# Kernel optimization log

Hardware: AMD Instinct MI355X
Metric: run time of the kernel (lower is better)

The kernel has to match this reference:

```python
import jax, jax.numpy as jnp
import numpy as np

B, N, S, D, ITERS = 128, 8192, 4, 32, 3
LN_EPS = 1e-5

def _ln(x, g, b):
    m = jnp.mean(x, axis=-1, keepdims=True)
    v = jnp.mean((x - m) ** 2, axis=-1, keepdims=True)
    return (x - m) * jax.lax.rsqrt(v + LN_EPS) * g + b

def setup_inputs() -> dict:
    key = jax.random.key(0)
    ks = jax.random.split(key, 16)
    s = 1.0 / np.sqrt(D)
    return {
        "x": jax.random.normal(ks[0], (B, N, D), jnp.float32),
        "slot_noise": jax.random.normal(ks[1], (B, S, D), jnp.float32),
        "slots_mu": jax.random.normal(ks[2], (1, 1, D), jnp.float32),
        "slots_logsigma": jnp.zeros((1, 1, D), jnp.float32),
        "Wq": jax.random.uniform(ks[3], (D, D), jnp.float32, -s, s),
        "Wk": jax.random.uniform(ks[4], (D, D), jnp.float32, -s, s),
        "Wv": jax.random.uniform(ks[5], (D, D), jnp.float32, -s, s),
        "gru_Wih": jax.random.uniform(ks[6], (3 * D, D), jnp.float32, -s, s),
        "gru_Whh": jax.random.uniform(ks[7], (3 * D, D), jnp.float32, -s, s),
        "gru_bih": jax.random.uniform(ks[8], (3 * D,), jnp.float32, -s, s),
        "gru_bhh": jax.random.uniform(ks[9], (3 * D,), jnp.float32, -s, s),
        "mlp_W1": jax.random.uniform(ks[10], (D, D), jnp.float32, -s, s),
        "mlp_b1": jax.random.uniform(ks[11], (D,), jnp.float32, -s, s),
        "mlp_W2": jax.random.uniform(ks[12], (D, D), jnp.float32, -s, s),
        "mlp_b2": jax.random.uniform(ks[13], (D,), jnp.float32, -s, s),
        "lnx_g": jnp.ones((D,), jnp.float32), "lnx_b": jnp.zeros((D,), jnp.float32),
        "lns_g": jnp.ones((D,), jnp.float32), "lns_b": jnp.zeros((D,), jnp.float32),
        "lnff_g": jnp.ones((D,), jnp.float32), "lnff_b": jnp.zeros((D,), jnp.float32),
    }

def reference(x, slot_noise, slots_mu, slots_logsigma, Wq, Wk, Wv,
              gru_Wih, gru_Whh, gru_bih, gru_bhh,
              mlp_W1, mlp_b1, mlp_W2, mlp_b2,
              lnx_g, lnx_b, lns_g, lns_b, lnff_g, lnff_b):
    d = x.shape[-1]
    scale = d ** (-0.5)
    xn = _ln(x, lnx_g, lnx_b)                      # [B,N,D]
    k = xn @ Wk.T                                  # [B,N,D] (x fixed -> hoist out of loop)
    v = xn @ Wv.T
    slots = slots_mu + slot_noise * jnp.exp(slots_logsigma)  # [B,S,D]
    for _ in range(ITERS):
        q = _ln(slots, lns_g, lns_b) @ Wq.T        # [B,S,D]
        attn = jnp.einsum('bsd,bnd->bsn', q, k) * scale
        attn = jax.nn.softmax(attn, axis=-1) + 1e-8
        attn = attn / jnp.sum(attn, axis=-1, keepdims=True)
        upd = jnp.einsum('bsn,bnd->bsd', attn, v)  # [B,S,D]
        # GRUCell (PyTorch gate order: r, z, n)
        gi = upd @ gru_Wih.T + gru_bih             # [B,S,3D]
        gh = slots @ gru_Whh.T + gru_bhh
        ir, iz, inn = jnp.split(gi, 3, axis=-1)
        hr, hz, hn = jnp.split(gh, 3, axis=-1)
        r = jax.nn.sigmoid(ir + hr)
        z = jax.nn.sigmoid(iz + hz)
        n = jnp.tanh(inn + r * hn)
        slots = (1.0 - z) * n + z * slots
        h = jax.nn.relu(_ln(slots, lnff_g, lnff_b) @ mlp_W1.T + mlp_b1)
        slots = slots + (h @ mlp_W2.T + mlp_b2)
    return slots.reshape(slots.shape[0], -1)
```

## Files before the change

### kernel.cpp

```cpp
#include <hip/hip_runtime.h>
#include <hip/hip_bf16.h>


#define Bn 128
#define Nn 8192
#define Sn 4
#define Dn 32
#define SCALE 0.17677669529663687f
#define RENORM (1.0f / (1.0f + (float)Nn * 1e-8f))

#define Cn 16
#define RPB (Nn / Cn)
#define PT 256
#define RSTEP (PT / 4)
#define NSTEP (RPB / RSTEP)

#define WS_REQ ((size_t)(16384 + 16384 + Bn*Cn*Sn*Dn + Bn*Cn*Sn + Bn*Cn*Sn) * 4)

__device__ __forceinline__ float sigmoidf_(float v) { return 1.0f / (1.0f + __expf(-v)); }

template<int CTRL>
__device__ __forceinline__ float dpp_xadd(float v) {
    int p = __builtin_amdgcn_update_dpp(0, __float_as_int(v), CTRL, 0xF, 0xF, true);
    return v + __int_as_float(p);
}
#define DPP_X1 0xB1
#define DPP_X2 0x4E

__global__ __launch_bounds__(128)
void init_kernel(const float* __restrict__ noise, const float* __restrict__ mu,
                 const float* __restrict__ logsig,
                 const float* __restrict__ lns_g, const float* __restrict__ lns_b,
                 const float* __restrict__ Wq, const float* __restrict__ Wk,
                 float* __restrict__ slots, float* __restrict__ qt)
{
    const int b = blockIdx.x;
    const int tid = threadIdx.x;
    const int s = tid >> 5, d = tid & 31;
    __shared__ float sh_a[4][32];
    __shared__ float sh_b[4][32];

    float sv = mu[d] + noise[(b * Sn + s) * Dn + d] * __expf(logsig[d]);
    slots[(b * Sn + s) * Dn + d] = sv;

    float sx = sv, sxx = sv * sv;
    #pragma unroll
    for (int m = 1; m <= 16; m <<= 1) { sx += __shfl_xor(sx, m); sxx += __shfl_xor(sxx, m); }
    float mean = sx * (1.0f / 32.0f);
    float var  = sxx * (1.0f / 32.0f) - mean * mean;
    sh_a[s][d] = (sv - mean) * rsqrtf(var + 1e-5f) * lns_g[d] + lns_b[d];
    __syncthreads();

    float q = 0.0f;
    #pragma unroll 8
    for (int j = 0; j < 32; ++j) q = fmaf(Wq[d * 32 + j], sh_a[s][j], q);
    sh_b[s][d] = q;
    __syncthreads();

    float qtv = 0.0f;
    #pragma unroll 8
    for (int i = 0; i < 32; ++i) qtv = fmaf(sh_b[s][i], Wk[i * 32 + d], qtv);
    qt[(b * Sn + s) * Dn + d] = qtv * SCALE;
}

__global__ __launch_bounds__(PT)
void pass_kernel(const float* __restrict__ x, const float* __restrict__ qt,
                 const float* __restrict__ lnx_g, const float* __restrict__ lnx_b,
                 float* __restrict__ part_pa, float* __restrict__ part_pb,
                 float* __restrict__ part_ps)
{
    const int c = blockIdx.x;
    const int b = blockIdx.y;
    const int tid = threadIdx.x;
    const int sub = tid & 3, col0 = sub * 8;
    const int rg  = tid >> 2;

    float qg[4][8], qgs[4], qe[4];
    {
        const float* qtb = qt + (size_t)b * Sn * Dn;
        float g8[8], e8[8];
        #pragma unroll
        for (int k = 0; k < 8; ++k) { g8[k] = lnx_g[col0 + k]; e8[k] = lnx_b[col0 + k]; }
        #pragma unroll
        for (int s = 0; s < 4; ++s) {
            float sg = 0.f, se = 0.f;
            #pragma unroll
            for (int k = 0; k < 8; ++k) {
                float q = qtb[s * Dn + col0 + k];
                qg[s][k] = q * g8[k];
                sg += qg[s][k];
                se = fmaf(q, e8[k], se);
            }
            sg = dpp_xadd<DPP_X1>(sg); sg = dpp_xadd<DPP_X2>(sg);
            se = dpp_xadd<DPP_X1>(se); se = dpp_xadd<DPP_X2>(se);
            qgs[s] = sg; qe[s] = se;
        }
    }

    float pa[4][8], pb[4] = {0.f,0.f,0.f,0.f}, ps[4] = {0.f,0.f,0.f,0.f};
    #pragma unroll
    for (int s = 0; s < 4; ++s)
        #pragma unroll
        for (int k = 0; k < 8; ++k) pa[s][k] = 0.f;

    const float* xb = x + ((size_t)b * Nn + (size_t)c * RPB) * Dn;
    const float* base = xb + (size_t)rg * Dn + col0;

    float4 v0  = *(const float4*)(base);
    float4 v1  = *(const float4*)(base + 4);
    float4 n10 = *(const float4*)(base + (size_t)RSTEP * Dn);
    float4 n11 = *(const float4*)(base + (size_t)RSTEP * Dn + 4);

    for (int t = 0; t < NSTEP; ++t) {
        const int t2 = (t + 2 < NSTEP) ? t + 2 : NSTEP - 1;
        const float* p2 = base + (size_t)(t2 * RSTEP) * Dn;
        float4 n20 = *(const float4*)(p2);
        float4 n21 = *(const float4*)(p2 + 4);

        float xv[8] = {v0.x, v0.y, v0.z, v0.w, v1.x, v1.y, v1.z, v1.w};

        float sx = 0.f, sxx = 0.f, ds[4] = {0.f,0.f,0.f,0.f};
        #pragma unroll
        for (int k = 0; k < 8; ++k) {
            sx += xv[k];
            sxx = fmaf(xv[k], xv[k], sxx);
            #pragma unroll
            for (int s = 0; s < 4; ++s) ds[s] = fmaf(xv[k], qg[s][k], ds[s]);
        }
        sx  = dpp_xadd<DPP_X1>(sx);   sx  = dpp_xadd<DPP_X2>(sx);
        sxx = dpp_xadd<DPP_X1>(sxx);  sxx = dpp_xadd<DPP_X2>(sxx);
        #pragma unroll
        for (int s = 0; s < 4; ++s) {
            ds[s] = dpp_xadd<DPP_X1>(ds[s]);
            ds[s] = dpp_xadd<DPP_X2>(ds[s]);
        }

        float mean = sx * (1.0f / 32.0f);
        float var  = sxx * (1.0f / 32.0f) - mean * mean;
        float rs   = rsqrtf(var + 1e-5f);

        #pragma unroll
        for (int s = 0; s < 4; ++s) {
            float tt = fmaf(-mean, qgs[s], ds[s]);
            float lg = fmaf(rs, tt, qe[s]);
            float w  = __expf(lg);
            float al = w * rs;
            ps[s] += w;
            pb[s] = fmaf(al, mean, pb[s]);
            #pragma unroll
            for (int k = 0; k < 8; ++k) pa[s][k] = fmaf(al, xv[k], pa[s][k]);
        }
        v0 = n10; v1 = n11; n10 = n20; n11 = n21;
    }

    #pragma unroll
    for (int m = 4; m <= 32; m <<= 1) {
        #pragma unroll
        for (int s = 0; s < 4; ++s) {
            ps[s] += __shfl_xor(ps[s], m);
            pb[s] += __shfl_xor(pb[s], m);
            #pragma unroll
            for (int k = 0; k < 8; ++k) pa[s][k] += __shfl_xor(pa[s][k], m);
        }
    }

    __shared__ float ls_pa[4][4][32];
    __shared__ float ls_pb[4][4];
    __shared__ float ls_ps[4][4];
    const int wv = tid >> 6, lane = tid & 63;
    if (lane < 4) {
        #pragma unroll
        for (int s = 0; s < 4; ++s)
            #pragma unroll
            for (int k = 0; k < 8; ++k) ls_pa[wv][s][lane * 8 + k] = pa[s][k];
        if (lane == 0) {
            #pragma unroll
            for (int s = 0; s < 4; ++s) { ls_pb[wv][s] = pb[s]; ls_ps[wv][s] = ps[s]; }
        }
    }
    __syncthreads();
    if (tid < 128) {
        const int s = tid >> 5, d = tid & 31;
        float a = ls_pa[0][s][d] + ls_pa[1][s][d] + ls_pa[2][s][d] + ls_pa[3][s][d];
        part_pa[(((size_t)b * Cn + c) * Sn + s) * Dn + d] = a;
        if (d == 0) {
            part_pb[((size_t)b * Cn + c) * Sn + s] =
                ls_pb[0][s] + ls_pb[1][s] + ls_pb[2][s] + ls_pb[3][s];
            part_ps[((size_t)b * Cn + c) * Sn + s] =
                ls_ps[0][s] + ls_ps[1][s] + ls_ps[2][s] + ls_ps[3][s];
        }
    }
}

__global__ __launch_bounds__(128)
void update_kernel(const float* __restrict__ part_pa, const float* __restrict__ part_pb,
                   const float* __restrict__ part_ps,
                   const float* __restrict__ lnx_g, const float* __restrict__ lnx_b,
                   const float* __restrict__ Wv,
                   const float* __restrict__ Wih, const float* __restrict__ Whh,
                   const float* __restrict__ bih, const float* __restrict__ bhh,
                   const float* __restrict__ W1, const float* __restrict__ b1v,
                   const float* __restrict__ W2, const float* __restrict__ b2v,
                   const float* __restrict__ lns_g, const float* __restrict__ lns_b,
                   const float* __restrict__ lnff_g, const float* __restrict__ lnff_b,
                   const float* __restrict__ Wq, const float* __restrict__ Wk,
                   float* __restrict__ slots, float* __restrict__ qt,
                   float* __restrict__ out, int write_out, int write_qt)
{
    const int b = blockIdx.x;
    const int tid = threadIdx.x;
    const int s = tid >> 5, d = tid & 31;
    __shared__ float sh_a[4][32];
    __shared__ float sh_b[4][32];
    __shared__ float sh_sold[4][32];
    __shared__ float sh_h[4][32];

    float PA = 0.f, PB = 0.f, PS = 0.f;
    #pragma unroll
    for (int c = 0; c < Cn; ++c) {
        PA += part_pa[(((size_t)b * Cn + c) * Sn + s) * Dn + d];
        PB += part_pb[((size_t)b * Cn + c) * Sn + s];
        PS += part_ps[((size_t)b * Cn + c) * Sn + s];
    }
    float u = fmaf(lnx_g[d], PA - PB, PS * lnx_b[d]);
    sh_a[s][d] = (u / PS) * RENORM;
    float sold = slots[(b * Sn + s) * Dn + d];
    sh_sold[s][d] = sold;
    __syncthreads();

    float upd = 0.f;
    #pragma unroll 8
    for (int j = 0; j < 32; ++j) upd = fmaf(Wv[d * 32 + j], sh_a[s][j], upd);
    sh_b[s][d] = upd;
    __syncthreads();

    float gi[3], gh[3];
    #pragma unroll
    for (int g3 = 0; g3 < 3; ++g3) {
        const int row = g3 * 32 + d;
        float a1 = bih[row], a2 = bhh[row];
        #pragma unroll 8
        for (int j = 0; j < 32; ++j) {
            a1 = fmaf(Wih[row * 32 + j], sh_b[s][j], a1);
            a2 = fmaf(Whh[row * 32 + j], sh_sold[s][j], a2);
        }
        gi[g3] = a1; gh[g3] = a2;
    }
    float r  = sigmoidf_(gi[0] + gh[0]);
    float z  = sigmoidf_(gi[1] + gh[1]);
    float nn = tanhf(gi[2] + r * gh[2]);
    float sv = (1.0f - z) * nn + z * sold;

    {
        float sx = sv, sxx = sv * sv;
        #pragma unroll
        for (int m = 1; m <= 16; m <<= 1) { sx += __shfl_xor(sx, m); sxx += __shfl_xor(sxx, m); }
        float mean = sx * (1.0f / 32.0f);
        float var  = sxx * (1.0f / 32.0f) - mean * mean;
        float rs   = rsqrtf(var + 1e-5f);
        __syncthreads();
        sh_a[s][d] = (sv - mean) * rs * lnff_g[d] + lnff_b[d];
    }
    __syncthreads();

    float h1 = b1v[d];
    #pragma unroll 8
    for (int j = 0; j < 32; ++j) h1 = fmaf(W1[d * 32 + j], sh_a[s][j], h1);
    sh_h[s][d] = fmaxf(h1, 0.0f);
    __syncthreads();

    float o = b2v[d];
    #pragma unroll 8
    for (int j = 0; j < 32; ++j) o = fmaf(W2[d * 32 + j], sh_h[s][j], o);
    float sfin = sv + o;

    slots[(b * Sn + s) * Dn + d] = sfin;
    if (write_out) out[(b * Sn + s) * Dn + d] = sfin;

    if (write_qt) {
        float sx = sfin, sxx = sfin * sfin;
        #pragma unroll
        for (int m = 1; m <= 16; m <<= 1) { sx += __shfl_xor(sx, m); sxx += __shfl_xor(sxx, m); }
        float mean = sx * (1.0f / 32.0f);
        float var  = sxx * (1.0f / 32.0f) - mean * mean;
        float rs   = rsqrtf(var + 1e-5f);
        __syncthreads();
        sh_a[s][d] = (sfin - mean) * rs * lns_g[d] + lns_b[d];
        __syncthreads();
        float q = 0.f;
        #pragma unroll 8
        for (int j = 0; j < 32; ++j) q = fmaf(Wq[d * 32 + j], sh_a[s][j], q);
        sh_b[s][d] = q;
        __syncthreads();
        float qtv = 0.f;
        #pragma unroll 8
        for (int i = 0; i < 32; ++i) qtv = fmaf(sh_b[s][i], Wk[i * 32 + d], qtv);
        qt[(b * Sn + s) * Dn + d] = qtv * SCALE;
    }
}

#define TPB 1024
#define NW (TPB / 64)
#define RPS (TPB / 4)
#define STEPS (Nn / RPS)

__global__ __launch_bounds__(TPB)
void slot_fused(const float* __restrict__ x, const float* __restrict__ noise,
                const float* __restrict__ mu, const float* __restrict__ logsig,
                const float* __restrict__ Wq, const float* __restrict__ Wk,
                const float* __restrict__ Wv,
                const float* __restrict__ Wih, const float* __restrict__ Whh,
                const float* __restrict__ bih, const float* __restrict__ bhh,
                const float* __restrict__ W1, const float* __restrict__ b1v,
                const float* __restrict__ W2, const float* __restrict__ b2v,
                const float* __restrict__ lnx_g, const float* __restrict__ lnx_b,
                const float* __restrict__ lns_g, const float* __restrict__ lns_b,
                const float* __restrict__ lnff_g, const float* __restrict__ lnff_b,
                float* __restrict__ out)
{
    const int b   = blockIdx.x;
    const int tid = threadIdx.x;
    __shared__ float slots_sh[Sn][Dn];
    __shared__ float qt_sh[Sn][Dn];
    __shared__ float a_sh[Sn][Dn];
    __shared__ float b_sh[Sn][Dn];
    __shared__ float h_sh[Sn][Dn];
    __shared__ float ls_u[NW][Sn][Dn];
    __shared__ float ls_s[NW][Sn];
    const int s128 = tid >> 5, d128 = tid & 31;

    if (tid < 128) {
        float sv = mu[d128] + noise[(b * Sn + s128) * Dn + d128] * __expf(logsig[d128]);
        slots_sh[s128][d128] = sv;
        float sx = sv, sxx = sv * sv;
        #pragma unroll
        for (int m = 1; m <= 16; m <<= 1) { sx += __shfl_xor(sx, m); sxx += __shfl_xor(sxx, m); }
        float mean = sx * (1.0f / 32.0f);
        float var  = sxx * (1.0f / 32.0f) - mean * mean;
        a_sh[s128][d128] = (sv - mean) * rsqrtf(var + 1e-5f) * lns_g[d128] + lns_b[d128];
    }
    __syncthreads();
    if (tid < 128) {
        float q = 0.f;
        #pragma unroll 8
        for (int j = 0; j < 32; ++j) q = fmaf(Wq[d128 * 32 + j], a_sh[s128][j], q);
        b_sh[s128][d128] = q;
    }
    __syncthreads();
    if (tid < 128) {
        float qv = 0.f;
        #pragma unroll 8
        for (int i = 0; i < 32; ++i) qv = fmaf(b_sh[s128][i], Wk[i * 32 + d128], qv);
        qt_sh[s128][d128] = qv * SCALE;
    }
    __syncthreads();

    const int sub = tid & 3, col0 = sub * 8;
    const int rg  = tid >> 2;
    float g_r[8], e_r[8];
    #pragma unroll
    for (int k = 0; k < 8; ++k) { g_r[k] = lnx_g[col0 + k]; e_r[k] = lnx_b[col0 + k]; }
    const float* xb = x + (size_t)b * Nn * Dn;
    float sv_reg = 0.f;

    for (int it = 0; it < 3; ++it) {
        float qt_r[4][8];
        #pragma unroll
        for (int s = 0; s < 4; ++s)
            #pragma unroll
            for (int k = 0; k < 8; ++k) qt_r[s][k] = qt_sh[s][col0 + k];
        float pu[4][8];
        float ps[4] = {0.f, 0.f, 0.f, 0.f};
        #pragma unroll
        for (int s = 0; s < 4; ++s)
            #pragma unroll
            for (int k = 0; k < 8; ++k) pu[s][k] = 0.f;

        const float* xr0 = xb + (size_t)rg * Dn + col0;
        float4 v0 = *(const float4*)(xr0);
        float4 v1 = *(const float4*)(xr0 + 4);
        #pragma unroll 2
        for (int t = 0; t < STEPS; ++t) {
            const float* xrn = xb + (size_t)((((t + 1) & (STEPS - 1)) * RPS) + rg) * Dn + col0;
            float4 n0 = *(const float4*)(xrn);
            float4 n1 = *(const float4*)(xrn + 4);
            float xv[8] = {v0.x, v0.y, v0.z, v0.w, v1.x, v1.y, v1.z, v1.w};
            float sx = 0.f, sxx = 0.f;
            #pragma unroll
            for (int k = 0; k < 8; ++k) { sx += xv[k]; sxx = fmaf(xv[k], xv[k], sxx); }
            sx += __shfl_xor(sx, 1); sxx += __shfl_xor(sxx, 1);
            sx += __shfl_xor(sx, 2); sxx += __shfl_xor(sxx, 2);
            float mean = sx * (1.0f / 32.0f);
            float var  = sxx * (1.0f / 32.0f) - mean * mean;
            float rs   = rsqrtf(var + 1e-5f);
            float xn[8];
            #pragma unroll
            for (int k = 0; k < 8; ++k) xn[k] = fmaf((xv[k] - mean) * rs, g_r[k], e_r[k]);
            #pragma unroll
            for (int s = 0; s < 4; ++s) {
                float a = 0.f;
                #pragma unroll
                for (int k = 0; k < 8; ++k) a = fmaf(xn[k], qt_r[s][k], a);
                a += __shfl_xor(a, 1);
                a += __shfl_xor(a, 2);
                float w = __expf(a);
                ps[s] += w;
                #pragma unroll
                for (int k = 0; k < 8; ++k) pu[s][k] = fmaf(w, xn[k], pu[s][k]);
            }
            v0 = n0; v1 = n1;
        }
        #pragma unroll
        for (int m = 4; m <= 32; m <<= 1) {
            #pragma unroll
            for (int s = 0; s < 4; ++s) {
                ps[s] += __shfl_xor(ps[s], m);
                #pragma unroll
                for (int k = 0; k < 8; ++k) pu[s][k] += __shfl_xor(pu[s][k], m);
            }
        }
        {
            const int wv = tid >> 6, lane = tid & 63;
            if (lane < 4) {
                #pragma unroll
                for (int s = 0; s < 4; ++s)
                    #pragma unroll
                    for (int k = 0; k < 8; ++k) ls_u[wv][s][lane * 8 + k] = pu[s][k];
                if (lane == 0) {
                    #pragma unroll
                    for (int s = 0; s < 4; ++s) ls_s[wv][s] = ps[s];
                }
            }
        }
        __syncthreads();
        if (tid < 128) {
            float u = 0.f, ss = 0.f;
            #pragma unroll
            for (int w = 0; w < NW; ++w) { u += ls_u[w][s128][d128]; ss += ls_s[w][s128]; }
            a_sh[s128][d128] = (u / ss) * RENORM;
        }
        __syncthreads();
        if (tid < 128) {
            float upd = 0.f;
            #pragma unroll 8
            for (int j = 0; j < 32; ++j) upd = fmaf(Wv[d128 * 32 + j], a_sh[s128][j], upd);
            b_sh[s128][d128] = upd;
        }
        __syncthreads();
        if (tid < 128) {
            float gi[3], gh[3];
            #pragma unroll
            for (int g3 = 0; g3 < 3; ++g3) {
                const int row = g3 * 32 + d128;
                float a1 = bih[row], a2 = bhh[row];
                #pragma unroll 8
                for (int j = 0; j < 32; ++j) {
                    a1 = fmaf(Wih[row * 32 + j], b_sh[s128][j], a1);
                    a2 = fmaf(Whh[row * 32 + j], slots_sh[s128][j], a2);
                }
                gi[g3] = a1; gh[g3] = a2;
            }
            float r  = sigmoidf_(gi[0] + gh[0]);
            float z  = sigmoidf_(gi[1] + gh[1]);
            float nn = tanhf(gi[2] + r * gh[2]);
            sv_reg = (1.0f - z) * nn + z * slots_sh[s128][d128];
            float sx = sv_reg, sxx = sv_reg * sv_reg;
            #pragma unroll
            for (int m = 1; m <= 16; m <<= 1) { sx += __shfl_xor(sx, m); sxx += __shfl_xor(sxx, m); }
            float mean = sx * (1.0f / 32.0f);
            float var  = sxx * (1.0f / 32.0f) - mean * mean;
            a_sh[s128][d128] = (sv_reg - mean) * rsqrtf(var + 1e-5f) * lnff_g[d128] + lnff_b[d128];
        }
        __syncthreads();
        if (tid < 128) {
            float h = b1v[d128];
            #pragma unroll 8
            for (int j = 0; j < 32; ++j) h = fmaf(W1[d128 * 32 + j], a_sh[s128][j], h);
            h_sh[s128][d128] = fmaxf(h, 0.f);
        }
        __syncthreads();
        if (tid < 128) {
            float o = b2v[d128];
            #pragma unroll 8
            for (int j = 0; j < 32; ++j) o = fmaf(W2[d128 * 32 + j], h_sh[s128][j], o);
            float sfin = sv_reg + o;
            slots_sh[s128][d128] = sfin;
            if (it < 2) {
                float sx = sfin, sxx = sfin * sfin;
                #pragma unroll
                for (int m = 1; m <= 16; m <<= 1) { sx += __shfl_xor(sx, m); sxx += __shfl_xor(sxx, m); }
                float mean = sx * (1.0f / 32.0f);
                float var  = sxx * (1.0f / 32.0f) - mean * mean;
                a_sh[s128][d128] = (sfin - mean) * rsqrtf(var + 1e-5f) * lns_g[d128] + lns_b[d128];
            }
        }
        __syncthreads();
        if (it < 2) {
            if (tid < 128) {
                float q = 0.f;
                #pragma unroll 8
                for (int j = 0; j < 32; ++j) q = fmaf(Wq[d128 * 32 + j], a_sh[s128][j], q);
                b_sh[s128][d128] = q;
            }
            __syncthreads();
            if (tid < 128) {
                float qv = 0.f;
                #pragma unroll 8
                for (int i = 0; i < 32; ++i) qv = fmaf(b_sh[s128][i], Wk[i * 32 + d128], qv);
                qt_sh[s128][d128] = qv * SCALE;
            }
            __syncthreads();
        }
    }
    if (tid < 128)
        out[(size_t)b * 128 + tid] = slots_sh[s128][d128];
}

extern "C" void kernel_launch(void* const* d_in, const int* in_sizes, int n_in,
                              void* d_out, int out_size, void* d_ws, size_t ws_size,
                              hipStream_t stream)
{
    const float* x      = (const float*)d_in[0];
    const float* noise  = (const float*)d_in[1];
    const float* mu     = (const float*)d_in[2];
    const float* logsig = (const float*)d_in[3];
    const float* Wq     = (const float*)d_in[4];
    const float* Wk     = (const float*)d_in[5];
    const float* Wv     = (const float*)d_in[6];
    const float* Wih    = (const float*)d_in[7];
    const float* Whh    = (const float*)d_in[8];
    const float* bih    = (const float*)d_in[9];
    const float* bhh    = (const float*)d_in[10];
    const float* W1     = (const float*)d_in[11];
    const float* b1v    = (const float*)d_in[12];
    const float* W2     = (const float*)d_in[13];
    const float* b2v    = (const float*)d_in[14];
    const float* lnx_g  = (const float*)d_in[15];
    const float* lnx_b  = (const float*)d_in[16];
    const float* lns_g  = (const float*)d_in[17];
    const float* lns_b  = (const float*)d_in[18];
    const float* lnff_g = (const float*)d_in[19];
    const float* lnff_b = (const float*)d_in[20];
    float* out = (float*)d_out;

    if (ws_size >= WS_REQ) {
        float* ws      = (float*)d_ws;
        float* slots   = ws;
        float* qt      = ws + 16384;
        float* part_pa = ws + 32768;
        float* part_pb = ws + 32768 + Bn * Cn * Sn * Dn;
        float* part_ps = part_pb + Bn * Cn * Sn;

        init_kernel<<<Bn, 128, 0, stream>>>(noise, mu, logsig, lns_g, lns_b, Wq, Wk,
                                            slots, qt);
        for (int it = 0; it < 3; ++it) {
            pass_kernel<<<dim3(Cn, Bn), PT, 0, stream>>>(x, qt, lnx_g, lnx_b,
                                                         part_pa, part_pb, part_ps);
            update_kernel<<<Bn, 128, 0, stream>>>(part_pa, part_pb, part_ps,
                                                  lnx_g, lnx_b, Wv, Wih, Whh, bih, bhh,
                                                  W1, b1v, W2, b2v, lns_g, lns_b,
                                                  lnff_g, lnff_b, Wq, Wk, slots, qt, out,
                                                  (it == 2) ? 1 : 0, (it < 2) ? 1 : 0);
        }
    } else {
        slot_fused<<<Bn, TPB, 0, stream>>>(x, noise, mu, logsig, Wq, Wk, Wv,
                                           Wih, Whh, bih, bhh, W1, b1v, W2, b2v,
                                           lnx_g, lnx_b, lns_g, lns_b, lnff_g, lnff_b,
                                           out);
    }
}
```

Baseline: 116.3 us.

## Cache layer-normed x as bf16 in workspace for later attention passes

The first pass now applies LayerNorm to x, stores the normalized rows as bf16 in a workspace buffer, and accumulates directly on the normalized values. The second and third passes read this half-size bf16 buffer instead of re-reading fp32 x and re-computing row statistics, and the pb correction term is dropped. This cuts HBM traffic for two of the three passes and simplifies the inner loop. The cost is an extra 64MB write in the first pass and bf16 rounding of the keys and values, which loosens accuracy.

```diff
diff --git a/kernel.cpp b/kernel.cpp
--- a/kernel.cpp
+++ b/kernel.cpp
@@ -15,7 +15,7 @@
 #define RSTEP (PT / 4)
 #define NSTEP (RPB / RSTEP)
 
-#define WS_REQ ((size_t)(16384 + 16384 + Bn*Cn*Sn*Dn + Bn*Cn*Sn + Bn*Cn*Sn) * 4)
+#define WS_REQ ((size_t)(16384 + 16384 + Bn*Cn*Sn*Dn + Bn*Cn*Sn) * 4 + (size_t)Bn * Nn * Dn * 2)
 
 __device__ __forceinline__ float sigmoidf_(float v) { return 1.0f / (1.0f + __expf(-v)); }
 
@@ -26,6 +26,14 @@
 }
 #define DPP_X1 0xB1
 #define DPP_X2 0x4E
+
+__device__ __forceinline__ unsigned f2bf_rne(float f) {
+    unsigned u = __float_as_uint(f);
+    u += 0x7fffu + ((u >> 16) & 1u);
+    return u >> 16;
+}
+__device__ __forceinline__ float bflo2f(unsigned u) { return __uint_as_float(u << 16); }
+__device__ __forceinline__ float bfhi2f(unsigned u) { return __uint_as_float(u & 0xffff0000u); }
 
 __global__ __launch_bounds__(128)
 void init_kernel(const float* __restrict__ noise, const float* __restrict__ mu,
@@ -63,11 +71,47 @@
     qt[(b * Sn + s) * Dn + d] = qtv * SCALE;
 }
 
+__device__ __forceinline__ void pass_epilogue(
+    int b, int c, int tid, float pa[4][8], float ps[4],
+    float (*ls_pa)[Sn][Dn], float (*ls_ps)[Sn],
+    float* __restrict__ pa_out, float* __restrict__ ps_out)
+{
+    #pragma unroll
+    for (int m = 4; m <= 32; m <<= 1) {
+        #pragma unroll
+        for (int s = 0; s < 4; ++s) {
+            ps[s] += __shfl_xor(ps[s], m);
+            #pragma unroll
+            for (int k = 0; k < 8; ++k) pa[s][k] += __shfl_xor(pa[s][k], m);
+        }
+    }
+    const int wv = tid >> 6, lane = tid & 63;
+    if (lane < 4) {
+        #pragma unroll
+        for (int s = 0; s < 4; ++s)
+            #pragma unroll
+            for (int k = 0; k < 8; ++k) ls_pa[wv][s][lane * 8 + k] = pa[s][k];
+        if (lane == 0) {
+            #pragma unroll
+            for (int s = 0; s < 4; ++s) ls_ps[wv][s] = ps[s];
+        }
+    }
+    __syncthreads();
+    if (tid < 128) {
+        const int s = tid >> 5, d = tid & 31;
+        float a = ls_pa[0][s][d] + ls_pa[1][s][d] + ls_pa[2][s][d] + ls_pa[3][s][d];
+        pa_out[(((size_t)b * Cn + c) * Sn + s) * Dn + d] = a;
+        if (d == 0)
+            ps_out[((size_t)b * Cn + c) * Sn + s] =
+                ls_ps[0][s] + ls_ps[1][s] + ls_ps[2][s] + ls_ps[3][s];
+    }
+}
+
 __global__ __launch_bounds__(PT)
-void pass_kernel(const float* __restrict__ x, const float* __restrict__ qt,
-                 const float* __restrict__ lnx_g, const float* __restrict__ lnx_b,
-                 float* __restrict__ part_pa, float* __restrict__ part_pb,
-                 float* __restrict__ part_ps)
+void pass0_kernel(const float* __restrict__ x, unsigned short* __restrict__ y,
+                  const float* __restrict__ qt,
+                  const float* __restrict__ lnx_g, const float* __restrict__ lnx_b,
+                  float* __restrict__ part_pa, float* __restrict__ part_ps)
 {
     const int c = blockIdx.x;
     const int b = blockIdx.y;
@@ -75,35 +119,25 @@
     const int sub = tid & 3, col0 = sub * 8;
     const int rg  = tid >> 2;
 
-    float qg[4][8], qgs[4], qe[4];
+    float qt_r[4][8], g_r[8], e_r[8];
     {
         const float* qtb = qt + (size_t)b * Sn * Dn;
-        float g8[8], e8[8];
-        #pragma unroll
-        for (int k = 0; k < 8; ++k) { g8[k] = lnx_g[col0 + k]; e8[k] = lnx_b[col0 + k]; }
-        #pragma unroll
-        for (int s = 0; s < 4; ++s) {
-            float sg = 0.f, se = 0.f;
-            #pragma unroll
-            for (int k = 0; k < 8; ++k) {
-                float q = qtb[s * Dn + col0 + k];
-                qg[s][k] = q * g8[k];
-                sg += qg[s][k];
-                se = fmaf(q, e8[k], se);
-            }
-            sg = dpp_xadd<DPP_X1>(sg); sg = dpp_xadd<DPP_X2>(sg);
-            se = dpp_xadd<DPP_X1>(se); se = dpp_xadd<DPP_X2>(se);
-            qgs[s] = sg; qe[s] = se;
-        }
-    }
-
-    float pa[4][8], pb[4] = {0.f,0.f,0.f,0.f}, ps[4] = {0.f,0.f,0.f,0.f};
+        #pragma unroll
+        for (int k = 0; k < 8; ++k) { g_r[k] = lnx_g[col0 + k]; e_r[k] = lnx_b[col0 + k]; }
+        #pragma unroll
+        for (int s = 0; s < 4; ++s)
+            #pragma unroll
+            for (int k = 0; k < 8; ++k) qt_r[s][k] = qtb[s * Dn + col0 + k];
+    }
+
+    float pa[4][8], ps[4] = {0.f,0.f,0.f,0.f};
     #pragma unroll
     for (int s = 0; s < 4; ++s)
         #pragma unroll
         for (int k = 0; k < 8; ++k) pa[s][k] = 0.f;
 
     const float* xb = x + ((size_t)b * Nn + (size_t)c * RPB) * Dn;
+    unsigned short* yb = y + ((size_t)b * Nn + (size_t)c * RPB) * Dn;
     const float* base = xb + (size_t)rg * Dn + col0;
 
     float4 v0  = *(const float4*)(base);
@@ -119,83 +153,119 @@
 
         float xv[8] = {v0.x, v0.y, v0.z, v0.w, v1.x, v1.y, v1.z, v1.w};
 
-        float sx = 0.f, sxx = 0.f, ds[4] = {0.f,0.f,0.f,0.f};
-        #pragma unroll
-        for (int k = 0; k < 8; ++k) {
-            sx += xv[k];
-            sxx = fmaf(xv[k], xv[k], sxx);
-            #pragma unroll
-            for (int s = 0; s < 4; ++s) ds[s] = fmaf(xv[k], qg[s][k], ds[s]);
-        }
+        float sx = 0.f, sxx = 0.f;
+        #pragma unroll
+        for (int k = 0; k < 8; ++k) { sx += xv[k]; sxx = fmaf(xv[k], xv[k], sxx); }
         sx  = dpp_xadd<DPP_X1>(sx);   sx  = dpp_xadd<DPP_X2>(sx);
         sxx = dpp_xadd<DPP_X1>(sxx);  sxx = dpp_xadd<DPP_X2>(sxx);
+        float mean = sx * (1.0f / 32.0f);
+        float var  = sxx * (1.0f / 32.0f) - mean * mean;
+        float rs   = rsqrtf(var + 1e-5f);
+
+        float xn[8];
+        #pragma unroll
+        for (int k = 0; k < 8; ++k) xn[k] = fmaf((xv[k] - mean) * rs, g_r[k], e_r[k]);
+
+        uint4 yw;
+        yw.x = (f2bf_rne(xn[1]) << 16) | f2bf_rne(xn[0]);
+        yw.y = (f2bf_rne(xn[3]) << 16) | f2bf_rne(xn[2]);
+        yw.z = (f2bf_rne(xn[5]) << 16) | f2bf_rne(xn[4]);
+        yw.w = (f2bf_rne(xn[7]) << 16) | f2bf_rne(xn[6]);
+        *(uint4*)(yb + (size_t)(t * RSTEP + rg) * Dn + col0) = yw;
+
+        float ds[4] = {0.f,0.f,0.f,0.f};
+        #pragma unroll
+        for (int k = 0; k < 8; ++k)
+            #pragma unroll
+            for (int s = 0; s < 4; ++s) ds[s] = fmaf(xn[k], qt_r[s][k], ds[s]);
         #pragma unroll
         for (int s = 0; s < 4; ++s) {
             ds[s] = dpp_xadd<DPP_X1>(ds[s]);
             ds[s] = dpp_xadd<DPP_X2>(ds[s]);
         }
-
-        float mean = sx * (1.0f / 32.0f);
-        float var  = sxx * (1.0f / 32.0f) - mean * mean;
-        float rs   = rsqrtf(var + 1e-5f);
-
         #pragma unroll
         for (int s = 0; s < 4; ++s) {
-            float tt = fmaf(-mean, qgs[s], ds[s]);
-            float lg = fmaf(rs, tt, qe[s]);
-            float w  = __expf(lg);
-            float al = w * rs;
+            float w = __expf(ds[s]);
             ps[s] += w;
-            pb[s] = fmaf(al, mean, pb[s]);
-            #pragma unroll
-            for (int k = 0; k < 8; ++k) pa[s][k] = fmaf(al, xv[k], pa[s][k]);
+            #pragma unroll
+            for (int k = 0; k < 8; ++k) pa[s][k] = fmaf(w, xn[k], pa[s][k]);
         }
         v0 = n10; v1 = n11; n10 = n20; n11 = n21;
     }
 
+    __shared__ float ls_pa[4][Sn][Dn];
+    __shared__ float ls_ps[4][Sn];
+    pass_epilogue(b, c, tid, pa, ps, ls_pa, ls_ps, part_pa, part_ps);
+}
+
+__global__ __launch_bounds__(PT)
+void pass12_kernel(const unsigned short* __restrict__ y, const float* __restrict__ qt,
+                   float* __restrict__ part_pa, float* __restrict__ part_ps)
+{
+    const int c = blockIdx.x;
+    const int b = blockIdx.y;
+    const int tid = threadIdx.x;
+    const int sub = tid & 3, col0 = sub * 8;
+    const int rg  = tid >> 2;
+
+    float qt_r[4][8];
+    {
+        const float* qtb = qt + (size_t)b * Sn * Dn;
+        #pragma unroll
+        for (int s = 0; s < 4; ++s)
+            #pragma unroll
+            for (int k = 0; k < 8; ++k) qt_r[s][k] = qtb[s * Dn + col0 + k];
+    }
+
+    float pa[4][8], ps[4] = {0.f,0.f,0.f,0.f};
     #pragma unroll
-    for (int m = 4; m <= 32; m <<= 1) {
+    for (int s = 0; s < 4; ++s)
+        #pragma unroll
+        for (int k = 0; k < 8; ++k) pa[s][k] = 0.f;
+
+    const unsigned short* yb = y + ((size_t)b * Nn + (size_t)c * RPB) * Dn;
+    const unsigned short* base = yb + (size_t)rg * Dn + col0;
+
+    uint4 v  = *(const uint4*)(base);
+    uint4 n1 = *(const uint4*)(base + (size_t)RSTEP * Dn);
+
+    for (int t = 0; t < NSTEP; ++t) {
+        const int t2 = (t + 2 < NSTEP) ? t + 2 : NSTEP - 1;
+        uint4 n2 = *(const uint4*)(base + (size_t)(t2 * RSTEP) * Dn);
+
+        float yv[8];
+        yv[0] = bflo2f(v.x); yv[1] = bfhi2f(v.x);
+        yv[2] = bflo2f(v.y); yv[3] = bfhi2f(v.y);
+        yv[4] = bflo2f(v.z); yv[5] = bfhi2f(v.z);
+        yv[6] = bflo2f(v.w); yv[7] = bfhi2f(v.w);
+
+        float ds[4] = {0.f,0.f,0.f,0.f};
+        #pragma unroll
+        for (int k = 0; k < 8; ++k)
+            #pragma unroll
+            for (int s = 0; s < 4; ++s) ds[s] = fmaf(yv[k], qt_r[s][k], ds[s]);
         #pragma unroll
         for (int s = 0; s < 4; ++s) {
-            ps[s] += __shfl_xor(ps[s], m);
-            pb[s] += __shfl_xor(pb[s], m);
-            #pragma unroll
-            for (int k = 0; k < 8; ++k) pa[s][k] += __shfl_xor(pa[s][k], m);
-        }
-    }
-
-    __shared__ float ls_pa[4][4][32];
-    __shared__ float ls_pb[4][4];
-    __shared__ float ls_ps[4][4];
-    const int wv = tid >> 6, lane = tid & 63;
-    if (lane < 4) {
-        #pragma unroll
-        for (int s = 0; s < 4; ++s)
-            #pragma unroll
-            for (int k = 0; k < 8; ++k) ls_pa[wv][s][lane * 8 + k] = pa[s][k];
-        if (lane == 0) {
-            #pragma unroll
-            for (int s = 0; s < 4; ++s) { ls_pb[wv][s] = pb[s]; ls_ps[wv][s] = ps[s]; }
-        }
-    }
-    __syncthreads();
-    if (tid < 128) {
-        const int s = tid >> 5, d = tid & 31;
-        float a = ls_pa[0][s][d] + ls_pa[1][s][d] + ls_pa[2][s][d] + ls_pa[3][s][d];
-        part_pa[(((size_t)b * Cn + c) * Sn + s) * Dn + d] = a;
-        if (d == 0) {
-            part_pb[((size_t)b * Cn + c) * Sn + s] =
-                ls_pb[0][s] + ls_pb[1][s] + ls_pb[2][s] + ls_pb[3][s];
-            part_ps[((size_t)b * Cn + c) * Sn + s] =
-                ls_ps[0][s] + ls_ps[1][s] + ls_ps[2][s] + ls_ps[3][s];
-        }
-    }
+            ds[s] = dpp_xadd<DPP_X1>(ds[s]);
+            ds[s] = dpp_xadd<DPP_X2>(ds[s]);
+        }
+        #pragma unroll
+        for (int s = 0; s < 4; ++s) {
+            float w = __expf(ds[s]);
+            ps[s] += w;
+            #pragma unroll
+            for (int k = 0; k < 8; ++k) pa[s][k] = fmaf(w, yv[k], pa[s][k]);
+        }
+        v = n1; n1 = n2;
+    }
+
+    __shared__ float ls_pa[4][Sn][Dn];
+    __shared__ float ls_ps[4][Sn];
+    pass_epilogue(b, c, tid, pa, ps, ls_pa, ls_ps, part_pa, part_ps);
 }
 
 __global__ __launch_bounds__(128)
-void update_kernel(const float* __restrict__ part_pa, const float* __restrict__ part_pb,
-                   const float* __restrict__ part_ps,
-                   const float* __restrict__ lnx_g, const float* __restrict__ lnx_b,
+void update_kernel(const float* __restrict__ part_pa, const float* __restrict__ part_ps,
                    const float* __restrict__ Wv,
                    const float* __restrict__ Wih, const float* __restrict__ Whh,
                    const float* __restrict__ bih, const float* __restrict__ bhh,
@@ -215,15 +285,13 @@
     __shared__ float sh_sold[4][32];
     __shared__ float sh_h[4][32];
 
-    float PA = 0.f, PB = 0.f, PS = 0.f;
+    float PA = 0.f, PS = 0.f;
     #pragma unroll
     for (int c = 0; c < Cn; ++c) {
         PA += part_pa[(((size_t)b * Cn + c) * Sn + s) * Dn + d];
-        PB += part_pb[((size_t)b * Cn + c) * Sn + s];
         PS += part_ps[((size_t)b * Cn + c) * Sn + s];
     }
-    float u = fmaf(lnx_g[d], PA - PB, PS * lnx_b[d]);
-    sh_a[s][d] = (u / PS) * RENORM;
+    sh_a[s][d] = (PA / PS) * RENORM;
     float sold = slots[(b * Sn + s) * Dn + d];
     sh_sold[s][d] = sold;
     __syncthreads();
@@ -548,20 +616,24 @@
         float* slots   = ws;
         float* qt      = ws + 16384;
         float* part_pa = ws + 32768;
-        float* part_pb = ws + 32768 + Bn * Cn * Sn * Dn;
-        float* part_ps = part_pb + Bn * Cn * Sn;
+        float* part_ps = part_pa + Bn * Cn * Sn * Dn;
+        unsigned short* ybuf = (unsigned short*)(part_ps + Bn * Cn * Sn);
 
         init_kernel<<<Bn, 128, 0, stream>>>(noise, mu, logsig, lns_g, lns_b, Wq, Wk,
                                             slots, qt);
-        for (int it = 0; it < 3; ++it) {
-            pass_kernel<<<dim3(Cn, Bn), PT, 0, stream>>>(x, qt, lnx_g, lnx_b,
-                                                         part_pa, part_pb, part_ps);
-            update_kernel<<<Bn, 128, 0, stream>>>(part_pa, part_pb, part_ps,
-                                                  lnx_g, lnx_b, Wv, Wih, Whh, bih, bhh,
-                                                  W1, b1v, W2, b2v, lns_g, lns_b,
-                                                  lnff_g, lnff_b, Wq, Wk, slots, qt, out,
-                                                  (it == 2) ? 1 : 0, (it < 2) ? 1 : 0);
-        }
+        pass0_kernel<<<dim3(Cn, Bn), PT, 0, stream>>>(x, ybuf, qt, lnx_g, lnx_b,
+                                                      part_pa, part_ps);
+        update_kernel<<<Bn, 128, 0, stream>>>(part_pa, part_ps, Wv, Wih, Whh, bih, bhh,
+                                              W1, b1v, W2, b2v, lns_g, lns_b,
+                                              lnff_g, lnff_b, Wq, Wk, slots, qt, out, 0, 1);
+        pass12_kernel<<<dim3(Cn, Bn), PT, 0, stream>>>(ybuf, qt, part_pa, part_ps);
+        update_kernel<<<Bn, 128, 0, stream>>>(part_pa, part_ps, Wv, Wih, Whh, bih, bhh,
+                                              W1, b1v, W2, b2v, lns_g, lns_b,
+                                              lnff_g, lnff_b, Wq, Wk, slots, qt, out, 0, 1);
+        pass12_kernel<<<dim3(Cn, Bn), PT, 0, stream>>>(ybuf, qt, part_pa, part_ps);
+        update_kernel<<<Bn, 128, 0, stream>>>(part_pa, part_ps, Wv, Wih, Whh, bih, bhh,
+                                              W1, b1v, W2, b2v, lns_g, lns_b,
+                                              lnff_g, lnff_b, Wq, Wk, slots, qt, out, 1, 0);
     } else {
         slot_fused<<<Bn, TPB, 0, stream>>>(x, noise, mu, logsig, Wq, Wk, Wv,
                                            Wih, Whh, bih, bhh, W1, b1v, W2, b2v,
```

After: 115.4 us. About the same (-0.7%).
